# Kernel tuning notes

Hardware: AMD Instinct MI355X
Metric: run time of the kernel (lower is better)

The kernel has to match this reference:

```python
import jax, jax.numpy as jnp
import numpy as np

B, S, D, H = 512, 64, 1024, 16  # seq_len=64 fixed by Reshape([-1,8,8,d_model])
DH = D // H


def setup_inputs() -> dict:
    key = jax.random.key(0)
    ks = jax.random.split(key, 5)
    w_scale = 0.02  # keep pre-softmax logits / activations in a sane range
    return {
        "x": jax.random.normal(ks[0], (B, S, D), jnp.float32),
        "wq_w": jax.random.normal(ks[1], (D, D), jnp.float32) * w_scale,
        "wq_b": jnp.zeros((D,), jnp.float32),
        "wk_w": jax.random.normal(ks[2], (D, D), jnp.float32) * w_scale,
        "wk_b": jnp.zeros((D,), jnp.float32),
        "wv_w": jax.random.normal(ks[3], (D, D), jnp.float32) * w_scale,
        "wv_b": jnp.zeros((D,), jnp.float32),
        "wo_w": jax.random.normal(ks[4], (D, D), jnp.float32) * w_scale,
        "wo_b": jnp.zeros((D,), jnp.float32),
    }


def _split_heads(t):
    # [B, S, D] -> [B, H, S, DH]
    b, s, _ = t.shape
    return t.reshape(b, s, H, DH).transpose(0, 2, 1, 3)


def reference(x, wq_w, wq_b, wk_w, wk_b, wv_w, wv_b, wo_w, wo_b):
    b, s, d = x.shape
    q = _split_heads(x @ wq_w + wq_b)
    k = _split_heads(x @ wk_w + wk_b)
    v = _split_heads(x @ wv_w + wv_b)
    # NOTE: original scales by sqrt(d_model), not sqrt(depth)
    scores = jnp.einsum("bhqd,bhkd->bhqk", q, k) / jnp.sqrt(jnp.float32(d))
    # original 'padding mask': (scores == 0) * 1e-9 added to scores
    scores = scores + (scores == 0).astype(scores.dtype) * 1e-9
    attn = jax.nn.softmax(scores, axis=-1)
    ctx = jnp.einsum("bhqk,bhkd->bhqd", attn, v)  # [B, H, S, DH]
    ctx = ctx.transpose(0, 2, 1, 3).reshape(b, s, d)  # [B, S, D]
    # keras Dense(..., activation='gelu') uses exact (erf) gelu by default
    out = jax.nn.gelu(ctx @ wo_w + wo_b, approximate=False)
    # Reshape([-1, 8, 8, D]) then squeeze -> [B, 8, 8, D]
    return out.reshape(b, 8, 8, d)
```

## Files before the change

kernel.cpp:

```cpp
#include <hip/hip_runtime.h>
#include <cstdint>
#include <math.h>

typedef float f32x4 __attribute__((ext_vector_type(4)));
typedef __bf16 bf16x8 __attribute__((ext_vector_type(8)));
typedef unsigned short u16x8 __attribute__((ext_vector_type(8)));
typedef unsigned short u16x4 __attribute__((ext_vector_type(4)));

typedef __attribute__((address_space(1))) const void* gas_cvptr;
typedef __attribute__((address_space(3))) void* las_vptr;

#define WAITV12 asm volatile("s_waitcnt vmcnt(12)" ::: "memory")
#define WAITV8 asm volatile("s_waitcnt vmcnt(8)" ::: "memory")
#define WAITV4 asm volatile("s_waitcnt vmcnt(4)" ::: "memory")
#define WAITV0 asm volatile("s_waitcnt vmcnt(0)" ::: "memory")
#define WAITL0 asm volatile("s_waitcnt lgkmcnt(0)" ::: "memory")
#define SB()   __builtin_amdgcn_sched_barrier(0)
#define BAR()  __builtin_amdgcn_s_barrier()

__device__ __forceinline__ unsigned short f32_to_bf16(float f) {
  uint32_t u = __builtin_bit_cast(uint32_t, f);
  u += 0x7FFFu + ((u >> 16) & 1u);
  return (unsigned short)(u >> 16);
}

__device__ __forceinline__ bf16x8 ld_bf16x8(const unsigned short* p) {
  return __builtin_bit_cast(bf16x8, *(const u16x8*)p);
}

__global__ void cvt_all(const float* __restrict__ x, unsigned short* __restrict__ xb, int n4,
                        const float* __restrict__ wq, const float* __restrict__ wk,
                        const float* __restrict__ wv, const float* __restrict__ wo,
                        unsigned short* __restrict__ wqkvT, unsigned short* __restrict__ woT) {
  __shared__ float tile[64][65];
  const int t = threadIdx.x;
  if (blockIdx.x < 1024) {
    const int z = blockIdx.x >> 8;
    const int rem = blockIdx.x & 255;
    const int by = rem >> 4, bx = rem & 15;
    const float* __restrict__ w = (z == 0) ? wq : (z == 1) ? wk : (z == 2) ? wv : wo;
    unsigned short* __restrict__ out = (z < 3) ? (wqkvT + (size_t)z * 1024 * 1024) : woT;
    const int r0 = by * 64;
    const int c0 = bx * 64;
#pragma unroll
    for (int i = 0; i < 4; i++) {
      int row = (t >> 4) + i * 16;
      int col = (t & 15) * 4;
      float4 v = *(const float4*)&w[(size_t)(r0 + row) * 1024 + c0 + col];
      tile[row][col] = v.x; tile[row][col + 1] = v.y;
      tile[row][col + 2] = v.z; tile[row][col + 3] = v.w;
    }
    __syncthreads();
#pragma unroll
    for (int i = 0; i < 2; i++) {
      int nr = (t >> 3) + i * 32;
      int kc = (t & 7) * 8;
      u16x8 o;
#pragma unroll
      for (int j = 0; j < 8; j++) o[j] = f32_to_bf16(tile[kc + j][nr]);
      *(u16x8*)&out[(size_t)(c0 + nr) * 1024 + r0 + kc] = o;
    }
  } else {
    const int nb = gridDim.x - 1024;
    const int stride = nb * blockDim.x;
    for (int i = (blockIdx.x - 1024) * blockDim.x + t; i < n4; i += stride) {
      float4 v = ((const float4*)x)[i];
      u16x4 o = { f32_to_bf16(v.x), f32_to_bf16(v.y), f32_to_bf16(v.z), f32_to_bf16(v.w) };
      ((u16x4*)xb)[i] = o;
    }
  }
}

struct Frags { bf16x8 afA[4], bfr[4], afB[4]; };

__device__ __forceinline__ void read_frags(Frags& f, const unsigned short* ab,
                                           const unsigned short* bb, int aRow0,
                                           int bRow0, int li, int koff) {
#pragma unroll
  for (int m = 0; m < 4; m++) f.afA[m] = ld_bf16x8(ab + (aRow0 + m * 16 + li) * 32 + koff);
#pragma unroll
  for (int n = 0; n < 4; n++) f.bfr[n] = ld_bf16x8(bb + (bRow0 + n * 16 + li) * 32 + koff);
#pragma unroll
  for (int m = 0; m < 4; m++)
    f.afB[m] = ld_bf16x8(ab + (aRow0 + 64 + m * 16 + li) * 32 + koff);
}

template <int EPI>
__global__ __launch_bounds__(512, 2) void gemm256(
    const unsigned short* __restrict__ A, const unsigned short* __restrict__ Bt,
    const float* __restrict__ b0, const float* __restrict__ b1, const float* __restrict__ b2,
    unsigned short* __restrict__ Qb, unsigned short* __restrict__ Kb, unsigned short* __restrict__ Vb,
    float* __restrict__ Out, int Ncols, int K) {
  __shared__ __align__(16) unsigned short As[4][256][32];
  __shared__ __align__(16) unsigned short Bs[4][256][32];
  const int NT = K >> 5;
  const int nb = Ncols >> 8;
  const int nwg = gridDim.x;
  const int cpx = nwg >> 3;
  const int bid = blockIdx.x;
  const int wg = (bid & 7) * cpx + (bid >> 3);
  const int tm = wg / nb, tn = wg % nb;
  const int rowBase = tm << 8, colBase = tn << 8;
  const int t = threadIdx.x;
  const int lane = t & 63;
  const int w = t >> 6;
  const int li = lane & 15, lg = lane >> 4;
  const int wm = w >> 2, wn = w & 3;
  const int aRow0 = wm * 128;
  const int bRow0 = wn * 64;
  const int koff = ((lg ^ ((li >> 1) & 3)) << 3);

  const int c0 = t, c1 = t + 512;
  const int r0s = c0 >> 2, r1s = c1 >> 2;
  const int l0s = (c0 & 3) ^ ((r0s >> 1) & 3);
  const int l1s = (c1 & 3) ^ ((r1s >> 1) & 3);
  const unsigned short* gA0 = A + (size_t)(rowBase + r0s) * K + l0s * 8;
  const unsigned short* gA1 = A + (size_t)(rowBase + r1s) * K + l1s * 8;
  const unsigned short* gB0 = Bt + (size_t)(colBase + r0s) * K + l0s * 8;
  const unsigned short* gB1 = Bt + (size_t)(colBase + r1s) * K + l1s * 8;

#define STAGE_AB(tile_) do { int b_ = (tile_) & 3; int kt_ = (tile_) << 5;                    \
    __builtin_amdgcn_global_load_lds((gas_cvptr)(gA0 + kt_),                                  \
        (las_vptr)(&As[b_][0][0] + c0 * 8), 16, 0, 0);                                        \
    __builtin_amdgcn_global_load_lds((gas_cvptr)(gA1 + kt_),                                  \
        (las_vptr)(&As[b_][0][0] + c1 * 8), 16, 0, 0);                                        \
    __builtin_amdgcn_global_load_lds((gas_cvptr)(gB0 + kt_),                                  \
        (las_vptr)(&Bs[b_][0][0] + c0 * 8), 16, 0, 0);                                        \
    __builtin_amdgcn_global_load_lds((gas_cvptr)(gB1 + kt_),                                  \
        (las_vptr)(&Bs[b_][0][0] + c1 * 8), 16, 0, 0); } while (0)

  STAGE_AB(0); STAGE_AB(1); STAGE_AB(2); STAGE_AB(3);
  WAITV12;
  BAR();

  f32x4 acc[8][4] = {};
  Frags F0, F1;
  read_frags(F0, &As[0][0][0], &Bs[0][0][0], aRow0, bRow0, li, koff);

#define TILE_BODY(tt_, CUR, NXT) do {                                                         \
    WAITL0; SB();                                                                             \
    __builtin_amdgcn_s_setprio(1);                                                            \
    _Pragma("unroll")                                                                         \
    for (int m = 0; m < 4; m++)                                                               \
      _Pragma("unroll")                                                                       \
      for (int n = 0; n < 4; n++)                                                             \
        acc[m][n] = __builtin_amdgcn_mfma_f32_16x16x32_bf16(CUR.afA[m], CUR.bfr[n],           \
                                                            acc[m][n], 0, 0, 0);              \
    __builtin_amdgcn_s_setprio(0);                                                            \
    if ((tt_) <= NT - 4)      WAITV8;                                                         \
    else if ((tt_) == NT - 3) WAITV4;                                                         \
    else if ((tt_) == NT - 2) WAITV0;                                                         \
    BAR();                                                                                    \
    if ((tt_) + 1 < NT)                                                                       \
      read_frags(NXT, &As[((tt_) + 1) & 3][0][0], &Bs[((tt_) + 1) & 3][0][0],                 \
                 aRow0, bRow0, li, koff);                                                     \
    if ((tt_) + 4 < NT) STAGE_AB((tt_) + 4);                                                  \
    __builtin_amdgcn_s_setprio(1);                                                            \
    _Pragma("unroll")                                                                         \
    for (int m = 0; m < 4; m++)                                                               \
      _Pragma("unroll")                                                                       \
      for (int n = 0; n < 4; n++)                                                             \
        acc[4 + m][n] = __builtin_amdgcn_mfma_f32_16x16x32_bf16(CUR.afB[m], CUR.bfr[n],       \
                                                                acc[4 + m][n], 0, 0, 0);      \
    __builtin_amdgcn_s_setprio(0);                                                            \
  } while (0)

  for (int tt = 0; tt < NT; tt += 2) {
    TILE_BODY(tt, F0, F1);
    TILE_BODY(tt + 1, F1, F0);
  }
#undef TILE_BODY
#undef STAGE_AB

  if (EPI == 0) {
    const int part = colBase >> 10;
    const float* __restrict__ bias = (part == 0) ? b0 : (part == 1) ? b1 : b2;
    unsigned short* __restrict__ dst = (part == 0) ? Qb : (part == 1) ? Kb : Vb;
#pragma unroll
    for (int mi = 0; mi < 8; mi++) {
      const int rowb = rowBase + aRow0 + mi * 16 + lg * 4;
#pragma unroll
      for (int r = 0; r < 4; r++) {
        const int row = rowb + r;
        const int b = row >> 6, s = row & 63;
#pragma unroll
        for (int n = 0; n < 4; n++) {
          const int col = colBase + bRow0 + n * 16 + li;
          const int within = col & 1023;
          const int h = within >> 6, dh = within & 63;
          float v = acc[mi][n][r] + bias[within];
          dst[(size_t)((b * 16 + h) * 64 + s) * 64 + dh] = f32_to_bf16(v);
        }
      }
    }
  } else {
#pragma unroll
    for (int mi = 0; mi < 8; mi++) {
      const int rowb = rowBase + aRow0 + mi * 16 + lg * 4;
#pragma unroll
      for (int r = 0; r < 4; r++) {
#pragma unroll
        for (int n = 0; n < 4; n++) {
          const int col = colBase + bRow0 + n * 16 + li;
          float v = acc[mi][n][r] + b0[col];
          v = 0.5f * v * (1.0f + erff(v * 0.70710678118654752f));
          Out[(size_t)(rowb + r) * 1024 + col] = v;
        }
      }
    }
  }
}

__global__ __launch_bounds__(256) void attn(
    const unsigned short* __restrict__ Qb, const unsigned short* __restrict__ Kb,
    const unsigned short* __restrict__ Vb, unsigned short* __restrict__ ctx) {
  __shared__ __align__(16) unsigned short Ks[64][72];
  __shared__ __align__(16) unsigned short Vt[64][72];
  __shared__ __align__(16) unsigned short Ps[64][72];
  const int bh = blockIdx.x;
  const int b = bh >> 4, h = bh & 15;
  const int t = threadIdx.x, lane = t & 63, w = t >> 6;
  const int li = lane & 15, lg = lane >> 4;
  const unsigned short* __restrict__ Qg = Qb + (size_t)bh * 4096;
  const unsigned short* __restrict__ Kg = Kb + (size_t)bh * 4096;
  const unsigned short* __restrict__ Vg = Vb + (size_t)bh * 4096;

  bf16x8 qa[2];
#pragma unroll
  for (int ks = 0; ks < 2; ks++)
    qa[ks] = ld_bf16x8(&Qg[(w * 16 + li) * 64 + ks * 32 + lg * 8]);

#pragma unroll
  for (int i = 0; i < 2; i++) {
    const int c = t + i * 256;
    const int row = c >> 3, col8 = (c & 7) * 8;
    *(u16x8*)&Ks[row][col8] = *(const u16x8*)&Kg[row * 64 + col8];
    u16x8 v = *(const u16x8*)&Vg[row * 64 + col8];
#pragma unroll
    for (int j = 0; j < 8; j++) Vt[col8 + j][row] = v[j];
  }
  __syncthreads();

  f32x4 sc[4] = {};
#pragma unroll
  for (int ks = 0; ks < 2; ks++) {
#pragma unroll
    for (int n = 0; n < 4; n++) {
      bf16x8 kf = ld_bf16x8(&Ks[n * 16 + li][ks * 32 + lg * 8]);
      sc[n] = __builtin_amdgcn_mfma_f32_16x16x32_bf16(qa[ks], kf, sc[n], 0, 0, 0);
    }
  }

#pragma unroll
  for (int r = 0; r < 4; r++) {
    float v0 = sc[0][r] * 0.03125f, v1 = sc[1][r] * 0.03125f;
    float v2 = sc[2][r] * 0.03125f, v3 = sc[3][r] * 0.03125f;
    float mx = fmaxf(fmaxf(v0, v1), fmaxf(v2, v3));
#pragma unroll
    for (int off = 1; off < 16; off <<= 1) mx = fmaxf(mx, __shfl_xor(mx, off, 64));
    float e0 = __expf(v0 - mx), e1 = __expf(v1 - mx);
    float e2 = __expf(v2 - mx), e3 = __expf(v3 - mx);
    float sum = e0 + e1 + e2 + e3;
#pragma unroll
    for (int off = 1; off < 16; off <<= 1) sum += __shfl_xor(sum, off, 64);
    float is = 1.0f / sum;
    const int q = w * 16 + lg * 4 + r;
    Ps[q][0 * 16 + li] = f32_to_bf16(e0 * is);
    Ps[q][1 * 16 + li] = f32_to_bf16(e1 * is);
    Ps[q][2 * 16 + li] = f32_to_bf16(e2 * is);
    Ps[q][3 * 16 + li] = f32_to_bf16(e3 * is);
  }

  f32x4 oc[4] = {};
#pragma unroll
  for (int ks = 0; ks < 2; ks++) {
    bf16x8 pa = ld_bf16x8(&Ps[w * 16 + li][ks * 32 + lg * 8]);
#pragma unroll
    for (int n = 0; n < 4; n++) {
      bf16x8 vf = ld_bf16x8(&Vt[n * 16 + li][ks * 32 + lg * 8]);
      oc[n] = __builtin_amdgcn_mfma_f32_16x16x32_bf16(pa, vf, oc[n], 0, 0, 0);
    }
  }
#pragma unroll
  for (int n = 0; n < 4; n++)
#pragma unroll
    for (int r = 0; r < 4; r++)
      ctx[(size_t)(b * 64 + w * 16 + lg * 4 + r) * 1024 + h * 64 + n * 16 + li] =
          f32_to_bf16(oc[n][r]);
}

extern "C" void kernel_launch(void* const* d_in, const int* in_sizes, int n_in,
                              void* d_out, int out_size, void* d_ws, size_t ws_size,
                              hipStream_t stream) {
  const float* x  = (const float*)d_in[0];
  const float* wq = (const float*)d_in[1];
  const float* bq = (const float*)d_in[2];
  const float* wk = (const float*)d_in[3];
  const float* bk = (const float*)d_in[4];
  const float* wv = (const float*)d_in[5];
  const float* bv = (const float*)d_in[6];
  const float* wo = (const float*)d_in[7];
  const float* bo = (const float*)d_in[8];
  float* out = (float*)d_out;

  const int D = 1024;
  const int M = in_sizes[0] / D;

  char* ws = (char*)d_ws;
  unsigned short* xb    = (unsigned short*)ws;
  unsigned short* wqkvT = (unsigned short*)(ws + (size_t)M * 1024 * 2);
  unsigned short* woT   = wqkvT + (size_t)3 * 1024 * 1024;
  unsigned short* Qb    = woT + (size_t)1024 * 1024;
  unsigned short* Kb    = Qb + (size_t)M * 1024;
  unsigned short* Vb    = Kb + (size_t)M * 1024;
  unsigned short* ctx   = xb;

  cvt_all<<<1024 + 2048, 256, 0, stream>>>(x, xb, M * D / 4, wq, wk, wv, wo, wqkvT, woT);
  gemm256<0><<<(M / 256) * (3072 / 256), 512, 0, stream>>>(
      xb, wqkvT, bq, bk, bv, Qb, Kb, Vb, nullptr, 3072, 1024);
  attn<<<(M / 64) * 16, 256, 0, stream>>>(Qb, Kb, Vb, ctx);
  gemm256<1><<<(M / 256) * (1024 / 256), 512, 0, stream>>>(
      ctx, woT, bo, nullptr, nullptr, nullptr, nullptr, nullptr, out, 1024, 1024);
}
```

Before: 406.5 us.

## Load GEMM A operand straight from global into registers, keep B in LDS

The GEMM no longer stages the A tile through LDS. Each wave loads its A fragments from global memory directly into registers one k-tile ahead, and only B still goes through LDS via global_load_lds, now with a 3-deep prefetch. This halves the LDS footprint and removes the A-side LDS reads and writes. In exchange, the four waves that share a row block each fetch the same A data from global/L2, and A's load latency is covered by only one tile of lookahead.

```diff
diff --git a/kernel.cpp b/kernel.cpp
--- a/kernel.cpp
+++ b/kernel.cpp
@@ -10,9 +10,7 @@
 typedef __attribute__((address_space(1))) const void* gas_cvptr;
 typedef __attribute__((address_space(3))) void* las_vptr;
 
-#define WAITV12 asm volatile("s_waitcnt vmcnt(12)" ::: "memory")
-#define WAITV8 asm volatile("s_waitcnt vmcnt(8)" ::: "memory")
-#define WAITV4 asm volatile("s_waitcnt vmcnt(4)" ::: "memory")
+#define WAITV2 asm volatile("s_waitcnt vmcnt(2)" ::: "memory")
 #define WAITV0 asm volatile("s_waitcnt vmcnt(0)" ::: "memory")
 #define WAITL0 asm volatile("s_waitcnt lgkmcnt(0)" ::: "memory")
 #define SB()   __builtin_amdgcn_sched_barrier(0)
@@ -71,19 +69,7 @@
   }
 }
 
-struct Frags { bf16x8 afA[4], bfr[4], afB[4]; };
-
-__device__ __forceinline__ void read_frags(Frags& f, const unsigned short* ab,
-                                           const unsigned short* bb, int aRow0,
-                                           int bRow0, int li, int koff) {
-#pragma unroll
-  for (int m = 0; m < 4; m++) f.afA[m] = ld_bf16x8(ab + (aRow0 + m * 16 + li) * 32 + koff);
-#pragma unroll
-  for (int n = 0; n < 4; n++) f.bfr[n] = ld_bf16x8(bb + (bRow0 + n * 16 + li) * 32 + koff);
-#pragma unroll
-  for (int m = 0; m < 4; m++)
-    f.afB[m] = ld_bf16x8(ab + (aRow0 + 64 + m * 16 + li) * 32 + koff);
-}
+struct AFrags { bf16x8 a[8]; };
 
 template <int EPI>
 __global__ __launch_bounds__(512, 2) void gemm256(
@@ -91,7 +77,6 @@
     const float* __restrict__ b0, const float* __restrict__ b1, const float* __restrict__ b2,
     unsigned short* __restrict__ Qb, unsigned short* __restrict__ Kb, unsigned short* __restrict__ Vb,
     float* __restrict__ Out, int Ncols, int K) {
-  __shared__ __align__(16) unsigned short As[4][256][32];
   __shared__ __align__(16) unsigned short Bs[4][256][32];
   const int NT = K >> 5;
   const int nb = Ncols >> 8;
@@ -110,67 +95,72 @@
   const int bRow0 = wn * 64;
   const int koff = ((lg ^ ((li >> 1) & 3)) << 3);
 
+  const unsigned short* __restrict__ aBase = A + (size_t)(rowBase + aRow0 + li) * K + lg * 8;
+
+#define LOAD_A(F, tt_) do { const unsigned short* p_ = aBase + ((tt_) << 5);                  \
+    _Pragma("unroll")                                                                         \
+    for (int m = 0; m < 4; m++) {                                                             \
+      (F).a[m]     = ld_bf16x8(p_ + (size_t)(m * 16) * K);                                    \
+      (F).a[4 + m] = ld_bf16x8(p_ + (size_t)(64 + m * 16) * K);                               \
+    } } while (0)
+
   const int c0 = t, c1 = t + 512;
   const int r0s = c0 >> 2, r1s = c1 >> 2;
   const int l0s = (c0 & 3) ^ ((r0s >> 1) & 3);
   const int l1s = (c1 & 3) ^ ((r1s >> 1) & 3);
-  const unsigned short* gA0 = A + (size_t)(rowBase + r0s) * K + l0s * 8;
-  const unsigned short* gA1 = A + (size_t)(rowBase + r1s) * K + l1s * 8;
   const unsigned short* gB0 = Bt + (size_t)(colBase + r0s) * K + l0s * 8;
   const unsigned short* gB1 = Bt + (size_t)(colBase + r1s) * K + l1s * 8;
 
-#define STAGE_AB(tile_) do { int b_ = (tile_) & 3; int kt_ = (tile_) << 5;                    \
-    __builtin_amdgcn_global_load_lds((gas_cvptr)(gA0 + kt_),                                  \
-        (las_vptr)(&As[b_][0][0] + c0 * 8), 16, 0, 0);                                        \
-    __builtin_amdgcn_global_load_lds((gas_cvptr)(gA1 + kt_),                                  \
-        (las_vptr)(&As[b_][0][0] + c1 * 8), 16, 0, 0);                                        \
+#define STAGE_B(tile_) do { int b_ = (tile_) & 3; int kt_ = (tile_) << 5;                     \
     __builtin_amdgcn_global_load_lds((gas_cvptr)(gB0 + kt_),                                  \
         (las_vptr)(&Bs[b_][0][0] + c0 * 8), 16, 0, 0);                                        \
     __builtin_amdgcn_global_load_lds((gas_cvptr)(gB1 + kt_),                                  \
         (las_vptr)(&Bs[b_][0][0] + c1 * 8), 16, 0, 0); } while (0)
 
-  STAGE_AB(0); STAGE_AB(1); STAGE_AB(2); STAGE_AB(3);
-  WAITV12;
+  STAGE_B(0); STAGE_B(1); STAGE_B(2);
+  AFrags A0, A1;
+  LOAD_A(A0, 0);
+  WAITV0;
   BAR();
 
   f32x4 acc[8][4] = {};
-  Frags F0, F1;
-  read_frags(F0, &As[0][0][0], &Bs[0][0][0], aRow0, bRow0, li, koff);
 
 #define TILE_BODY(tt_, CUR, NXT) do {                                                         \
+    if ((tt_) <= NT - 3) { WAITV2; } else { WAITV0; }                                         \
+    bf16x8 bfr[4];                                                                            \
+    const unsigned short* bb_ = &Bs[(tt_) & 3][0][0];                                         \
+    _Pragma("unroll")                                                                         \
+    for (int n = 0; n < 4; n++)                                                               \
+      bfr[n] = ld_bf16x8(bb_ + (bRow0 + n * 16 + li) * 32 + koff);                            \
     WAITL0; SB();                                                                             \
     __builtin_amdgcn_s_setprio(1);                                                            \
     _Pragma("unroll")                                                                         \
     for (int m = 0; m < 4; m++)                                                               \
       _Pragma("unroll")                                                                       \
       for (int n = 0; n < 4; n++)                                                             \
-        acc[m][n] = __builtin_amdgcn_mfma_f32_16x16x32_bf16(CUR.afA[m], CUR.bfr[n],           \
+        acc[m][n] = __builtin_amdgcn_mfma_f32_16x16x32_bf16(CUR.a[m], bfr[n],                 \
                                                             acc[m][n], 0, 0, 0);              \
     __builtin_amdgcn_s_setprio(0);                                                            \
-    if ((tt_) <= NT - 4)      WAITV8;                                                         \
-    else if ((tt_) == NT - 3) WAITV4;                                                         \
-    else if ((tt_) == NT - 2) WAITV0;                                                         \
     BAR();                                                                                    \
-    if ((tt_) + 1 < NT)                                                                       \
-      read_frags(NXT, &As[((tt_) + 1) & 3][0][0], &Bs[((tt_) + 1) & 3][0][0],                 \
-                 aRow0, bRow0, li, koff);                                                     \
-    if ((tt_) + 4 < NT) STAGE_AB((tt_) + 4);                                                  \
+    if ((tt_) + 1 < NT) LOAD_A(NXT, (tt_) + 1);                                               \
+    if ((tt_) + 3 < NT) STAGE_B((tt_) + 3);                                                   \
     __builtin_amdgcn_s_setprio(1);                                                            \
     _Pragma("unroll")                                                                         \
     for (int m = 0; m < 4; m++)                                                               \
       _Pragma("unroll")                                                                       \
       for (int n = 0; n < 4; n++)                                                             \
-        acc[4 + m][n] = __builtin_amdgcn_mfma_f32_16x16x32_bf16(CUR.afB[m], CUR.bfr[n],       \
+        acc[4 + m][n] = __builtin_amdgcn_mfma_f32_16x16x32_bf16(CUR.a[4 + m], bfr[n],         \
                                                                 acc[4 + m][n], 0, 0, 0);      \
     __builtin_amdgcn_s_setprio(0);                                                            \
   } while (0)
 
   for (int tt = 0; tt < NT; tt += 2) {
-    TILE_BODY(tt, F0, F1);
-    TILE_BODY(tt + 1, F1, F0);
+    TILE_BODY(tt, A0, A1);
+    TILE_BODY(tt + 1, A1, A0);
   }
 #undef TILE_BODY
-#undef STAGE_AB
+#undef STAGE_B
+#undef LOAD_A
 
   if (EPI == 0) {
     const int part = colBase >> 10;
```

Result: slower. 728.5 us (+79.2%).
